# Optimization experiments

Hardware: AMD Instinct MI355X
Metric: run time of the kernel (lower is better)

The kernel has to match this reference:

```python
import jax, jax.numpy as jnp
import numpy as np

DIM = 4096
N_HEAD = 32
N_KV_HEAD = 8
HEAD_DIM = DIM // N_HEAD  # 128
B, T = 2, 2048


def _rope_freqs(T, head_dim, theta=10000.0):
    inv = 1.0 / (theta ** (np.arange(0, head_dim, 2, dtype=np.float32) / head_dim))
    t = np.arange(T, dtype=np.float32)
    ang = np.outer(t, inv)  # [T, head_dim/2]
    return jnp.asarray(np.stack([np.cos(ang), np.sin(ang)], axis=-1))  # [T, hd/2, 2]


def setup_inputs() -> dict:
    key = jax.random.key(0)
    ks = jax.random.split(key, 5)
    s = 1.0 / np.sqrt(DIM)
    return {
        "x": jax.random.normal(ks[0], (B, T, DIM), dtype=jnp.float32),
        "freqs_cis": _rope_freqs(T, HEAD_DIM),
        "wq": jax.random.normal(ks[1], (DIM, N_HEAD * HEAD_DIM), dtype=jnp.float32) * s,
        "wk": jax.random.normal(ks[2], (DIM, N_KV_HEAD * HEAD_DIM), dtype=jnp.float32) * s,
        "wv": jax.random.normal(ks[3], (DIM, N_KV_HEAD * HEAD_DIM), dtype=jnp.float32) * s,
        "wo": jax.random.normal(ks[4], (DIM, DIM), dtype=jnp.float32) * s,
    }


def _apply_rotary(x, freqs_cis):
    # x: [B, T, H, head_dim]; freqs_cis: [T, head_dim/2, 2]
    xs = x.reshape(*x.shape[:-1], -1, 2)  # [B, T, H, hd/2, 2]
    fc = freqs_cis[None, :, None, :, :]   # [1, T, 1, hd/2, 2]
    real = xs[..., 0] * fc[..., 0] - xs[..., 1] * fc[..., 1]
    imag = xs[..., 1] * fc[..., 0] + xs[..., 0] * fc[..., 1]
    return jnp.stack([real, imag], axis=-1).reshape(x.shape)


def reference(x, freqs_cis, wq, wk, wv, wo):
    Bx, Tx, C = x.shape
    q = (x @ wq).reshape(Bx, Tx, N_HEAD, HEAD_DIM)
    k = (x @ wk).reshape(Bx, Tx, N_KV_HEAD, HEAD_DIM)
    v = (x @ wv).reshape(Bx, Tx, N_KV_HEAD, HEAD_DIM)
    q = _apply_rotary(q, freqs_cis)
    k = _apply_rotary(k, freqs_cis)
    # [B, H, T, hd]
    q = q.transpose(0, 2, 1, 3)
    k = k.transpose(0, 2, 1, 3)
    v = v.transpose(0, 2, 1, 3)
    # GQA: expand kv heads to match query heads
    rep = N_HEAD // N_KV_HEAD
    k = jnp.repeat(k, rep, axis=1)
    v = jnp.repeat(v, rep, axis=1)
    scale = 1.0 / np.sqrt(HEAD_DIM)
    scores = jnp.einsum("bhqd,bhkd->bhqk", q, k) * scale
    causal = jnp.tril(jnp.ones((Tx, Tx), dtype=bool))
    scores = jnp.where(causal[None, None], scores, jnp.float32(-1e30))
    attn = jax.nn.softmax(scores, axis=-1)
    y = jnp.einsum("bhqk,bhkd->bhqd", attn, v)
    y = y.transpose(0, 2, 1, 3).reshape(Bx, Tx, C)
    return y @ wo
```

## Files before the change

### kernel.cpp

```cpp
#include <hip/hip_runtime.h>

#define DIM  4096
#define NH   32
#define NKV  8
#define HD   128
#define BSZ  2
#define TSEQ 2048

typedef __bf16 bf16x8 __attribute__((ext_vector_type(8)));
typedef unsigned short ushort8v __attribute__((ext_vector_type(8)));
typedef float f32x4 __attribute__((ext_vector_type(4)));

typedef void GV __attribute__((address_space(1)));
typedef void LV __attribute__((address_space(3)));

__device__ __forceinline__ unsigned short f2bf(float f) {
  unsigned u = __builtin_bit_cast(unsigned, f);
  u += 0x7FFFu + ((u >> 16) & 1u);
  return (unsigned short)(u >> 16);
}
__device__ __forceinline__ float bf2f(unsigned short b) {
  unsigned u = ((unsigned)b) << 16;
  return __builtin_bit_cast(float, u);
}
__device__ __forceinline__ void gload16(const unsigned short* g, unsigned short* l) {
  __builtin_amdgcn_global_load_lds((GV*)g, (LV*)l, 16, 0, 0);
}
__device__ __forceinline__ f32x4 mfma16(bf16x8 a, bf16x8 b, f32x4 c) {
  return __builtin_amdgcn_mfma_f32_16x16x32_bf16(a, b, c, 0, 0, 0);
}
__device__ __forceinline__ bf16x8 lds8(const unsigned short* p) {
  return __builtin_bit_cast(bf16x8, *(const ushort8v*)p);
}

__global__ void detect_dtype(const unsigned int* __restrict__ fc, int* __restrict__ flag) {
  if (threadIdx.x == 0 && blockIdx.x == 0)
    *flag = (fc[0] == 0x3F800000u) ? 0 : 1;
}

__global__ void cast_x(const void* __restrict__ src, unsigned short* __restrict__ dst,
                       const int* __restrict__ flag) {
  long t = (long)blockIdx.x * 256 + threadIdx.x;
  if (*flag) {
    ((uint2*)dst)[t] = ((const uint2*)src)[t];
  } else {
    float4 f = ((const float4*)src)[t];
    ushort4 o;
    o.x = f2bf(f.x); o.y = f2bf(f.y); o.z = f2bf(f.z); o.w = f2bf(f.w);
    ((ushort4*)dst)[t] = o;
  }
}

__global__ __launch_bounds__(256) void transpose64(const void* __restrict__ src,
                                                   unsigned short* __restrict__ dst,
                                                   int R, int C, const int* __restrict__ flag) {
  __shared__ unsigned short tile[64][68];
  const int isbf = *flag;
  const int tid = threadIdx.x;
  const int c0g = blockIdx.x * 64, r0g = blockIdx.y * 64;
  const int cc = (tid & 15) * 4;
  if (isbf) {
    const unsigned short* s = (const unsigned short*)src;
#pragma unroll
    for (int it = 0; it < 4; ++it) {
      const int r = it * 16 + (tid >> 4);
      ushort4 v = *(const ushort4*)(s + (long)(r0g + r) * C + c0g + cc);
      *(ushort4*)&tile[r][cc] = v;
    }
  } else {
    const float* s = (const float*)src;
#pragma unroll
    for (int it = 0; it < 4; ++it) {
      const int r = it * 16 + (tid >> 4);
      float4 f = *(const float4*)(s + (long)(r0g + r) * C + c0g + cc);
      ushort4 v;
      v.x = f2bf(f.x); v.y = f2bf(f.y); v.z = f2bf(f.z); v.w = f2bf(f.w);
      *(ushort4*)&tile[r][cc] = v;
    }
  }
  __syncthreads();
#pragma unroll
  for (int it = 0; it < 2; ++it) {
    const int c = (tid >> 3) + it * 32;
    const int r0 = (tid & 7) * 8;
    ushort8v o;
#pragma unroll
    for (int u = 0; u < 8; ++u) o[u] = tile[r0 + u][c];
    *(ushort8v*)(dst + (long)(c0g + c) * R + r0g + r0) = o;
  }
}

__device__ __forceinline__ void gemm256_loop(const unsigned short* __restrict__ A,
                                             const unsigned short* __restrict__ Bt,
                                             unsigned short* As, unsigned short* Bs,
                                             long tileM, long tileN, f32x4 (&acc)[8][4]) {
  const int tid = (int)threadIdx.x;
  const int lane = tid & 63, wave = tid >> 6;
  const int wr = wave >> 2, wc = wave & 3;
  const int lm = lane & 15, quad = lane >> 4;
  const int srow = wave * 8 + (lane >> 3);
  const int schunk = ((lane & 7) ^ (lane >> 3)) * 8;
  const unsigned short* Ag = A + (tileM + srow) * 4096L + schunk;
  const unsigned short* Bg = Bt + (tileN + srow) * 4096L + schunk;
  unsigned short* Al = As + srow * 64 + (lane & 7) * 8;
  unsigned short* Bl = Bs + srow * 64 + (lane & 7) * 8;

  auto stgA = [&](int slot, int h, int tt) {
    const unsigned short* g = Ag + (long)h * 524288L + (long)tt * 64;
    unsigned short* l = Al + slot * 16384 + h * 8192;
    gload16(g, l);
    gload16(g + 262144L, l + 4096);
  };
  auto stgB = [&](int slot, int h, int tt) {
    const unsigned short* g = Bg + (long)h * 524288L + (long)tt * 64;
    unsigned short* l = Bl + slot * 16384 + h * 8192;
    gload16(g, l);
    gload16(g + 262144L, l + 4096);
  };
  auto rdA = [&](int so, int f16, int kk) {
    return lds8(&As[so + (wr * 128 + f16 * 16 + lm) * 64 + (((kk * 4 + quad) ^ (lm & 7)) * 8)]);
  };
  auto rdB = [&](int so, int f16, int kk) {
    return lds8(&Bs[so + (wc * 64 + f16 * 16 + lm) * 64 + (((kk * 4 + quad) ^ (lm & 7)) * 8)]);
  };

  stgB(0, 0, 0); stgB(0, 1, 0); stgA(0, 0, 0); stgA(0, 1, 0);
  stgB(1, 0, 1); stgB(1, 1, 1); stgA(1, 0, 1);
  asm volatile("s_waitcnt vmcnt(6)" ::: "memory");
  __builtin_amdgcn_sched_barrier(0);
  __builtin_amdgcn_s_barrier();
  __builtin_amdgcn_sched_barrier(0);

#pragma unroll 2
  for (int t = 0; t < 64; ++t) {
    const int s = t & 1;
    const int so = s * 16384;
    bf16x8 a[4][2], b[4][2];
#pragma unroll
    for (int f = 0; f < 4; ++f) { a[f][0] = rdA(so, f, 0); a[f][1] = rdA(so, f, 1); }
#pragma unroll
    for (int f = 0; f < 4; ++f) { b[f][0] = rdB(so, f, 0); b[f][1] = rdB(so, f, 1); }
    if (t < 63) stgA(s ^ 1, 1, t + 1);
    __builtin_amdgcn_sched_barrier(0);
    __builtin_amdgcn_s_barrier();
    asm volatile("s_waitcnt lgkmcnt(0)" ::: "memory");
    __builtin_amdgcn_sched_barrier(0);
    __builtin_amdgcn_s_setprio(1);
#pragma unroll
    for (int mf = 0; mf < 4; ++mf)
#pragma unroll
      for (int nf = 0; nf < 2; ++nf) {
        acc[mf][nf] = mfma16(a[mf][0], b[nf][0], acc[mf][nf]);
        acc[mf][nf] = mfma16(a[mf][1], b[nf][1], acc[mf][nf]);
      }
    __builtin_amdgcn_s_setprio(0);
    __builtin_amdgcn_sched_barrier(0);
    __builtin_amdgcn_s_barrier();
    if (t < 62) stgB(s, 0, t + 2);
    __builtin_amdgcn_sched_barrier(0);
    __builtin_amdgcn_s_barrier();
    __builtin_amdgcn_sched_barrier(0);
    __builtin_amdgcn_s_setprio(1);
#pragma unroll
    for (int mf = 0; mf < 4; ++mf)
#pragma unroll
      for (int nf = 2; nf < 4; ++nf) {
        acc[mf][nf] = mfma16(a[mf][0], b[nf][0], acc[mf][nf]);
        acc[mf][nf] = mfma16(a[mf][1], b[nf][1], acc[mf][nf]);
      }
    __builtin_amdgcn_s_setprio(0);
    __builtin_amdgcn_sched_barrier(0);
    __builtin_amdgcn_s_barrier();
#pragma unroll
    for (int f = 0; f < 4; ++f) { a[f][0] = rdA(so, f + 4, 0); a[f][1] = rdA(so, f + 4, 1); }
    if (t < 62) stgB(s, 1, t + 2);
    __builtin_amdgcn_sched_barrier(0);
    __builtin_amdgcn_s_barrier();
    asm volatile("s_waitcnt lgkmcnt(0)" ::: "memory");
    __builtin_amdgcn_sched_barrier(0);
    __builtin_amdgcn_s_setprio(1);
#pragma unroll
    for (int mf = 0; mf < 4; ++mf)
#pragma unroll
      for (int nf = 0; nf < 2; ++nf) {
        acc[mf + 4][nf] = mfma16(a[mf][0], b[nf][0], acc[mf + 4][nf]);
        acc[mf + 4][nf] = mfma16(a[mf][1], b[nf][1], acc[mf + 4][nf]);
      }
    __builtin_amdgcn_s_setprio(0);
    __builtin_amdgcn_sched_barrier(0);
    __builtin_amdgcn_s_barrier();
    if (t < 62) stgA(s, 0, t + 2);
    __builtin_amdgcn_sched_barrier(0);
    __builtin_amdgcn_s_barrier();
    __builtin_amdgcn_sched_barrier(0);
    __builtin_amdgcn_s_setprio(1);
#pragma unroll
    for (int mf = 0; mf < 4; ++mf)
#pragma unroll
      for (int nf = 2; nf < 4; ++nf) {
        acc[mf + 4][nf] = mfma16(a[mf][0], b[nf][0], acc[mf + 4][nf]);
        acc[mf + 4][nf] = mfma16(a[mf][1], b[nf][1], acc[mf + 4][nf]);
      }
    __builtin_amdgcn_s_setprio(0);
    if (t < 62)       asm volatile("s_waitcnt vmcnt(6)" ::: "memory");
    else if (t == 62) asm volatile("s_waitcnt vmcnt(0)" ::: "memory");
    __builtin_amdgcn_sched_barrier(0);
    __builtin_amdgcn_s_barrier();
  }
}

__global__ __launch_bounds__(512, 2) void gemm_qkv8(const unsigned short* __restrict__ A,
                                                    const unsigned short* __restrict__ Bt,
                                                    const void* __restrict__ fcv,
                                                    const int* __restrict__ flag,
                                                    unsigned short* __restrict__ qo,
                                                    unsigned short* __restrict__ ko,
                                                    unsigned short* __restrict__ vo) {
  __shared__ __align__(16) unsigned short As[2 * 16384];
  __shared__ __align__(16) unsigned short Bs[2 * 16384];
  const int bid = (int)blockIdx.x;
  const int nb2 = (bid & 7) * 48 + (bid >> 3);
  const long tileM = (long)(nb2 / 24) * 256;
  const long tileN = (long)(nb2 % 24) * 256;
  f32x4 acc[8][4] = {};
  gemm256_loop(A, Bt, As, Bs, tileM, tileN, acc);
  const int tid = (int)threadIdx.x;
  const int lane = tid & 63, wave = tid >> 6;
  const int wr = wave >> 2, wc = wave & 3;
  const int lm = lane & 15, quad = lane >> 4;
  const int isbf = *flag;
  const int nb = (int)tileN + wc * 64;
  if (nb < 5120) {
    const int isk = (nb >= 4096);
    unsigned short* dst = isk ? ko : qo;
    const int hpb = isk ? NKV : NH;
    const int coff = isk ? 4096 : 0;
#pragma unroll
    for (int mf = 0; mf < 8; ++mf)
#pragma unroll
      for (int r = 0; r < 4; ++r) {
        const int m = (int)tileM + wr * 128 + mf * 16 + quad * 4 + r;
        const int b = m >> 11, tq = m & (TSEQ - 1);
#pragma unroll
        for (int nf = 0; nf < 4; ++nf) {
          const int n = nb + nf * 16 + lm;
          float val = acc[mf][nf][r];
          float par = __shfl_xor(val, 1);
          const int ip = (n & 127) >> 1;
          const long fo = (long)tq * 64 + ip;
          float cz, sz;
          if (isbf) {
            const unsigned short* fu = (const unsigned short*)fcv;
            cz = bf2f(fu[fo * 2]); sz = bf2f(fu[fo * 2 + 1]);
          } else {
            float2 cs = ((const float2*)fcv)[fo];
            cz = cs.x; sz = cs.y;
          }
          float out = (n & 1) ? (val * cz + par * sz) : (val * cz - par * sz);
          const int h = (n - coff) >> 7, d = n & 127;
          dst[((long)(b * hpb + h) * TSEQ + tq) * HD + d] = f2bf(out);
        }
      }
  } else {
#pragma unroll
    for (int mf = 0; mf < 8; ++mf)
#pragma unroll
      for (int r = 0; r < 4; ++r) {
        const int m = (int)tileM + wr * 128 + mf * 16 + quad * 4 + r;
        const int b = m >> 11, tq = m & (TSEQ - 1);
#pragma unroll
        for (int nf = 0; nf < 4; ++nf) {
          const int n = nb + nf * 16 + lm;
          const int h = (n - 5120) >> 7, d = n & 127;
          vo[((long)(b * NKV + h) * HD + d) * TSEQ + tq] = f2bf(acc[mf][nf][r]);
        }
      }
  }
}

__global__ __launch_bounds__(512, 2) void gemm_wo8(const unsigned short* __restrict__ A,
                                                   const unsigned short* __restrict__ Bt,
                                                   void* __restrict__ Cv,
                                                   const int* __restrict__ flag) {
  __shared__ __align__(16) unsigned short As[2 * 16384];
  __shared__ __align__(16) unsigned short Bs[2 * 16384];
  const int bid = (int)blockIdx.x;
  const int nb2 = (bid & 7) * 32 + (bid >> 3);
  const long tileM = (long)(nb2 >> 4) * 256;
  const long tileN = (long)(nb2 & 15) * 256;
  f32x4 acc[8][4] = {};
  gemm256_loop(A, Bt, As, Bs, tileM, tileN, acc);
  const int tid = (int)threadIdx.x;
  const int lane = tid & 63, wave = tid >> 6;
  const int wr = wave >> 2, wc = wave & 3;
  const int lm = lane & 15, quad = lane >> 4;
  const int obf = *flag;
  const long N = 4096;
  if (obf) {
    unsigned short* C = (unsigned short*)Cv;
#pragma unroll
    for (int mf = 0; mf < 8; ++mf)
#pragma unroll
      for (int nf = 0; nf < 4; ++nf)
#pragma unroll
        for (int r = 0; r < 4; ++r)
          C[(tileM + wr * 128 + mf * 16 + quad * 4 + r) * N + tileN + wc * 64 + nf * 16 + lm] =
              f2bf(acc[mf][nf][r]);
  } else {
    float* C = (float*)Cv;
#pragma unroll
    for (int mf = 0; mf < 8; ++mf)
#pragma unroll
      for (int nf = 0; nf < 4; ++nf)
#pragma unroll
        for (int r = 0; r < 4; ++r)
          C[(tileM + wr * 128 + mf * 16 + quad * 4 + r) * N + tileN + wc * 64 + nf * 16 + lm] =
              acc[mf][nf][r];
  }
}

__global__ __launch_bounds__(256, 3) void flash_attn(const unsigned short* __restrict__ q,
                                                     const unsigned short* __restrict__ k,
                                                     const unsigned short* __restrict__ vT,
                                                     unsigned short* __restrict__ y) {
  __shared__ unsigned short Ks[2][32 * 128];
  __shared__ unsigned short Vs[2][128 * 32];
  __shared__ unsigned short Pl[4][32 * 40];
  const int tid = threadIdx.x;
  const int lane = tid & 63, wave = tid >> 6;
  const int lm = lane & 15, quad = lane >> 4;
  const int bh = blockIdx.y, b = bh >> 5, h = bh & 31, kvh = h >> 2;
  const int qi = (int)gridDim.x - 1 - (int)blockIdx.x;
  const int q0 = qi * 128;
  const unsigned short* Qb = q + ((long)(b * NH + h) * TSEQ + q0 + wave * 32) * HD;
  const unsigned short* Kb = k + (long)(b * NKV + kvh) * TSEQ * HD;
  const unsigned short* Vb = vT + (long)(b * NKV + kvh) * HD * TSEQ;
  bf16x8 qf[2][4];
#pragma unroll
  for (int mi = 0; mi < 2; ++mi)
#pragma unroll
    for (int ks = 0; ks < 4; ++ks)
      qf[mi][ks] = __builtin_bit_cast(bf16x8,
          *(const ushort8v*)(Qb + (mi * 16 + lm) * HD + ks * 32 + quad * 8));
  f32x4 o[2][8] = {};
  float li[2][4] = {};
  const float scale = 0.08838834764831845f;
  const int krow = tid >> 4, kcl = ((tid & 15) ^ (krow & 7)) * 8;
  const int vrow = tid >> 2, vcl = ((tid & 3) ^ ((vrow >> 1) & 3)) * 8;
  const int ktiles = qi * 4 + 4;
  {
    gload16(Kb + krow * HD + kcl, &Ks[0][tid * 8]);
    gload16(Kb + (16 + krow) * HD + kcl, &Ks[0][2048 + tid * 8]);
    gload16(Vb + (long)vrow * TSEQ + vcl, &Vs[0][tid * 8]);
    gload16(Vb + (long)(64 + vrow) * TSEQ + vcl, &Vs[0][2048 + tid * 8]);
  }
  for (int kt = 0; kt < ktiles; ++kt) {
    __syncthreads();
    if (kt + 1 < ktiles) {
      const int bi = (kt + 1) & 1;
      const unsigned short* Kg = Kb + (long)(kt + 1) * 32 * HD;
      gload16(Kg + krow * HD + kcl, &Ks[bi][tid * 8]);
      gload16(Kg + (16 + krow) * HD + kcl, &Ks[bi][2048 + tid * 8]);
      const unsigned short* Vg = Vb + (kt + 1) * 32;
      gload16(Vg + (long)vrow * TSEQ + vcl, &Vs[bi][tid * 8]);
      gload16(Vg + (long)(64 + vrow) * TSEQ + vcl, &Vs[bi][2048 + tid * 8]);
    }
    const unsigned short* KsB = Ks[kt & 1];
    const unsigned short* VsB = Vs[kt & 1];
    f32x4 s[2][2] = {};
#pragma unroll
    for (int ni = 0; ni < 2; ++ni)
#pragma unroll
      for (int ks = 0; ks < 4; ++ks) {
        bf16x8 kf = lds8(&KsB[(ni * 16 + lm) * 128 + ((ks * 4 + quad) ^ (lm & 7)) * 8]);
        s[0][ni] = mfma16(qf[0][ks], kf, s[0][ni]);
        s[1][ni] = mfma16(qf[1][ks], kf, s[1][ni]);
      }
    unsigned short* PlW = &Pl[wave][0];
#pragma unroll
    for (int mi = 0; mi < 2; ++mi)
#pragma unroll
      for (int r = 0; r < 4; ++r) {
        const int qg = q0 + wave * 32 + mi * 16 + quad * 4 + r;
#pragma unroll
        for (int ni = 0; ni < 2; ++ni) {
          const int kg = kt * 32 + ni * 16 + lm;
          float p = (kg <= qg) ? __expf(s[mi][ni][r] * scale) : 0.f;
          li[mi][r] += p;
          PlW[(mi * 16 + quad * 4 + r) * 40 + ni * 16 + lm] = f2bf(p);
        }
      }
    bf16x8 pf0 = lds8(&PlW[lm * 40 + quad * 8]);
    bf16x8 pf1 = lds8(&PlW[(16 + lm) * 40 + quad * 8]);
#pragma unroll
    for (int db = 0; db < 8; ++db) {
      bf16x8 vf = lds8(&VsB[(db * 16 + lm) * 32 + (quad ^ ((lm >> 1) & 3)) * 8]);
      o[0][db] = mfma16(pf0, vf, o[0][db]);
      o[1][db] = mfma16(pf1, vf, o[1][db]);
    }
  }
  float inv[2][4];
#pragma unroll
  for (int mi = 0; mi < 2; ++mi)
#pragma unroll
    for (int r = 0; r < 4; ++r) {
      float l = li[mi][r];
      l += __shfl_xor(l, 1, 16);
      l += __shfl_xor(l, 2, 16);
      l += __shfl_xor(l, 4, 16);
      l += __shfl_xor(l, 8, 16);
      inv[mi][r] = 1.0f / l;
    }
  unsigned short* yo = y + ((long)b * TSEQ + q0 + wave * 32) * DIM + h * 128 + lm;
#pragma unroll
  for (int mi = 0; mi < 2; ++mi)
#pragma unroll
    for (int r = 0; r < 4; ++r) {
      unsigned short* yr = yo + (long)(mi * 16 + quad * 4 + r) * DIM;
#pragma unroll
      for (int db = 0; db < 8; ++db)
        yr[db * 16] = f2bf(o[mi][db][r] * inv[mi][r]);
    }
}

extern "C" void kernel_launch(void* const* d_in, const int* in_sizes, int n_in,
                              void* d_out, int out_size, void* d_ws, size_t ws_size,
                              hipStream_t stream) {
  const void* x  = d_in[0];
  const void* fc = d_in[1];
  const void* wq = d_in[2];
  const void* wk = d_in[3];
  const void* wv = d_in[4];
  const void* wo = d_in[5];
  char* ws = (char*)d_ws;
  int* flag             = (int*)ws;
  unsigned short* xb    = (unsigned short*)(ws + 256);
  unsigned short* wqkvT = xb + 16777216L;
  unsigned short* woT   = wqkvT + 25165824L;
  unsigned short* qb    = woT + 16777216L;
  unsigned short* kb    = qb + 16777216L;
  unsigned short* vb    = kb + 4194304L;
  unsigned short* yb    = xb;

  detect_dtype<<<dim3(1), dim3(64), 0, stream>>>((const unsigned int*)fc, flag);
  cast_x<<<dim3(16384), dim3(256), 0, stream>>>(x, xb, flag);
  transpose64<<<dim3(64, 64), dim3(256), 0, stream>>>(wq, wqkvT, 4096, 4096, flag);
  transpose64<<<dim3(16, 64), dim3(256), 0, stream>>>(wk, wqkvT + 4096L * 4096, 4096, 1024, flag);
  transpose64<<<dim3(16, 64), dim3(256), 0, stream>>>(wv, wqkvT + 5120L * 4096, 4096, 1024, flag);
  transpose64<<<dim3(64, 64), dim3(256), 0, stream>>>(wo, woT, 4096, 4096, flag);
  gemm_qkv8<<<dim3(384), dim3(512), 0, stream>>>(xb, wqkvT, fc, flag, qb, kb, vb);
  flash_attn<<<dim3(16, 64), dim3(256), 0, stream>>>(qb, kb, vb, yb);
  gemm_wo8<<<dim3(256), dim3(512), 0, stream>>>(yb, woT, d_out, flag);
}
```

Measured before the change: 831.5 us.

## Split B-fragment LDS reads across quadrants and drop sched barriers in QKV GEMM loop

Reworks the main GEMM k-loop so the B fragments are read from LDS in two halves, each just before the MFMA quadrant that uses it. The global stage of B-half-1 and A-half-0 is merged into a single phase. Explicit lgkmcnt waits and most sched_barrier fences are removed, leaving the compiler to insert waits and schedule freely. The aim is to overlap LDS reads with MFMA work and cut register pressure and barrier overhead. The risk is that the compiler's scheduling is worse than the hand-fenced version.

```diff
diff --git a/kernel.cpp b/kernel.cpp
--- a/kernel.cpp
+++ b/kernel.cpp
@@ -127,84 +127,70 @@
   stgB(0, 0, 0); stgB(0, 1, 0); stgA(0, 0, 0); stgA(0, 1, 0);
   stgB(1, 0, 1); stgB(1, 1, 1); stgA(1, 0, 1);
   asm volatile("s_waitcnt vmcnt(6)" ::: "memory");
-  __builtin_amdgcn_sched_barrier(0);
   __builtin_amdgcn_s_barrier();
-  __builtin_amdgcn_sched_barrier(0);
 
 #pragma unroll 2
   for (int t = 0; t < 64; ++t) {
+    __builtin_amdgcn_sched_barrier(0);
     const int s = t & 1;
     const int so = s * 16384;
-    bf16x8 a[4][2], b[4][2];
+    bf16x8 a[4][2], b0[2][2], b1[2][2];
 #pragma unroll
     for (int f = 0; f < 4; ++f) { a[f][0] = rdA(so, f, 0); a[f][1] = rdA(so, f, 1); }
 #pragma unroll
-    for (int f = 0; f < 4; ++f) { b[f][0] = rdB(so, f, 0); b[f][1] = rdB(so, f, 1); }
+    for (int f = 0; f < 2; ++f) { b0[f][0] = rdB(so, f, 0); b0[f][1] = rdB(so, f, 1); }
     if (t < 63) stgA(s ^ 1, 1, t + 1);
-    __builtin_amdgcn_sched_barrier(0);
-    __builtin_amdgcn_s_barrier();
-    asm volatile("s_waitcnt lgkmcnt(0)" ::: "memory");
-    __builtin_amdgcn_sched_barrier(0);
+    __builtin_amdgcn_s_barrier();
     __builtin_amdgcn_s_setprio(1);
 #pragma unroll
     for (int mf = 0; mf < 4; ++mf)
 #pragma unroll
       for (int nf = 0; nf < 2; ++nf) {
-        acc[mf][nf] = mfma16(a[mf][0], b[nf][0], acc[mf][nf]);
-        acc[mf][nf] = mfma16(a[mf][1], b[nf][1], acc[mf][nf]);
+        acc[mf][nf] = mfma16(a[mf][0], b0[nf][0], acc[mf][nf]);
+        acc[mf][nf] = mfma16(a[mf][1], b0[nf][1], acc[mf][nf]);
       }
     __builtin_amdgcn_s_setprio(0);
-    __builtin_amdgcn_sched_barrier(0);
-    __builtin_amdgcn_s_barrier();
+    __builtin_amdgcn_s_barrier();
+#pragma unroll
+    for (int f = 0; f < 2; ++f) { b1[f][0] = rdB(so, f + 2, 0); b1[f][1] = rdB(so, f + 2, 1); }
+    __builtin_amdgcn_s_barrier();
+    __builtin_amdgcn_s_setprio(1);
+#pragma unroll
+    for (int mf = 0; mf < 4; ++mf)
+#pragma unroll
+      for (int nf = 0; nf < 2; ++nf) {
+        acc[mf][nf + 2] = mfma16(a[mf][0], b1[nf][0], acc[mf][nf + 2]);
+        acc[mf][nf + 2] = mfma16(a[mf][1], b1[nf][1], acc[mf][nf + 2]);
+      }
+    __builtin_amdgcn_s_setprio(0);
+    __builtin_amdgcn_s_barrier();
+#pragma unroll
+    for (int f = 0; f < 4; ++f) { a[f][0] = rdA(so, f + 4, 0); a[f][1] = rdA(so, f + 4, 1); }
     if (t < 62) stgB(s, 0, t + 2);
-    __builtin_amdgcn_sched_barrier(0);
-    __builtin_amdgcn_s_barrier();
-    __builtin_amdgcn_sched_barrier(0);
+    __builtin_amdgcn_s_barrier();
     __builtin_amdgcn_s_setprio(1);
 #pragma unroll
     for (int mf = 0; mf < 4; ++mf)
 #pragma unroll
-      for (int nf = 2; nf < 4; ++nf) {
-        acc[mf][nf] = mfma16(a[mf][0], b[nf][0], acc[mf][nf]);
-        acc[mf][nf] = mfma16(a[mf][1], b[nf][1], acc[mf][nf]);
+      for (int nf = 0; nf < 2; ++nf) {
+        acc[mf + 4][nf] = mfma16(a[mf][0], b0[nf][0], acc[mf + 4][nf]);
+        acc[mf + 4][nf] = mfma16(a[mf][1], b0[nf][1], acc[mf + 4][nf]);
       }
     __builtin_amdgcn_s_setprio(0);
-    __builtin_amdgcn_sched_barrier(0);
-    __builtin_amdgcn_s_barrier();
-#pragma unroll
-    for (int f = 0; f < 4; ++f) { a[f][0] = rdA(so, f + 4, 0); a[f][1] = rdA(so, f + 4, 1); }
-    if (t < 62) stgB(s, 1, t + 2);
-    __builtin_amdgcn_sched_barrier(0);
-    __builtin_amdgcn_s_barrier();
-    asm volatile("s_waitcnt lgkmcnt(0)" ::: "memory");
-    __builtin_amdgcn_sched_barrier(0);
+    __builtin_amdgcn_s_barrier();
+    if (t < 62) { stgB(s, 1, t + 2); stgA(s, 0, t + 2); }
+    __builtin_amdgcn_s_barrier();
     __builtin_amdgcn_s_setprio(1);
 #pragma unroll
     for (int mf = 0; mf < 4; ++mf)
 #pragma unroll
       for (int nf = 0; nf < 2; ++nf) {
-        acc[mf + 4][nf] = mfma16(a[mf][0], b[nf][0], acc[mf + 4][nf]);
-        acc[mf + 4][nf] = mfma16(a[mf][1], b[nf][1], acc[mf + 4][nf]);
-      }
-    __builtin_amdgcn_s_setprio(0);
-    __builtin_amdgcn_sched_barrier(0);
-    __builtin_amdgcn_s_barrier();
-    if (t < 62) stgA(s, 0, t + 2);
-    __builtin_amdgcn_sched_barrier(0);
-    __builtin_amdgcn_s_barrier();
-    __builtin_amdgcn_sched_barrier(0);
-    __builtin_amdgcn_s_setprio(1);
-#pragma unroll
-    for (int mf = 0; mf < 4; ++mf)
-#pragma unroll
-      for (int nf = 2; nf < 4; ++nf) {
-        acc[mf + 4][nf] = mfma16(a[mf][0], b[nf][0], acc[mf + 4][nf]);
-        acc[mf + 4][nf] = mfma16(a[mf][1], b[nf][1], acc[mf + 4][nf]);
+        acc[mf + 4][nf + 2] = mfma16(a[mf][0], b1[nf][0], acc[mf + 4][nf + 2]);
+        acc[mf + 4][nf + 2] = mfma16(a[mf][1], b1[nf][1], acc[mf + 4][nf + 2]);
       }
     __builtin_amdgcn_s_setprio(0);
     if (t < 62)       asm volatile("s_waitcnt vmcnt(6)" ::: "memory");
     else if (t == 62) asm volatile("s_waitcnt vmcnt(0)" ::: "memory");
-    __builtin_amdgcn_sched_barrier(0);
     __builtin_amdgcn_s_barrier();
   }
 }
```

Measured after the change: 846.0 us. Within noise of the previous version (+1.7%).

## Shrink GEMM tiles from 256x256 to 128x128 with 4-wave blocks

Applied to the files above, without the earlier changes.

Replaces the 256x256, 512-thread GEMM main loop with a 128x128, 256-thread version and halves the LDS buffers. The QKV and output projection GEMMs now launch four times as many blocks, and the block-index swizzles and epilogue indexing are updated to match. The aim is better CU occupancy and load balance (384/256 blocks on a 256-CU part). The cost is lower arithmetic intensity per tile, so more global and LDS traffic per FLOP, plus more barriers per MFMA.

```diff
diff --git a/kernel.cpp b/kernel.cpp
--- a/kernel.cpp
+++ b/kernel.cpp
@@ -90,38 +90,38 @@
   }
 }
 
-__device__ __forceinline__ void gemm256_loop(const unsigned short* __restrict__ A,
+__device__ __forceinline__ void gemm128_loop(const unsigned short* __restrict__ A,
                                              const unsigned short* __restrict__ Bt,
                                              unsigned short* As, unsigned short* Bs,
-                                             long tileM, long tileN, f32x4 (&acc)[8][4]) {
+                                             long tileM, long tileN, f32x4 (&acc)[4][4]) {
   const int tid = (int)threadIdx.x;
   const int lane = tid & 63, wave = tid >> 6;
-  const int wr = wave >> 2, wc = wave & 3;
+  const int wr = wave >> 1, wc = wave & 1;
   const int lm = lane & 15, quad = lane >> 4;
-  const int srow = wave * 8 + (lane >> 3);
-  const int schunk = ((lane & 7) ^ (lane >> 3)) * 8;
-  const unsigned short* Ag = A + (tileM + srow) * 4096L + schunk;
-  const unsigned short* Bg = Bt + (tileN + srow) * 4096L + schunk;
-  unsigned short* Al = As + srow * 64 + (lane & 7) * 8;
-  unsigned short* Bl = Bs + srow * 64 + (lane & 7) * 8;
-
-  auto stgA = [&](int slot, int h, int tt) {
-    const unsigned short* g = Ag + (long)h * 524288L + (long)tt * 64;
-    unsigned short* l = Al + slot * 16384 + h * 8192;
+  const int sr = tid >> 3;
+  const int schunk = ((tid & 7) ^ (sr & 7)) * 8;
+  const unsigned short* Ag = A + (tileM + sr) * 4096L + schunk;
+  const unsigned short* Bg = Bt + (tileN + sr) * 4096L + schunk;
+  unsigned short* Al = As + sr * 64 + (tid & 7) * 8;
+  unsigned short* Bl = Bs + sr * 64 + (tid & 7) * 8;
+
+  auto stgA = [&](int slot, int half, int tt) {
+    const unsigned short* g = Ag + (long)half * (64 * 4096L) + (long)tt * 64;
+    unsigned short* l = Al + slot * 8192 + half * 4096;
     gload16(g, l);
-    gload16(g + 262144L, l + 4096);
+    gload16(g + 32 * 4096L, l + 2048);
   };
-  auto stgB = [&](int slot, int h, int tt) {
-    const unsigned short* g = Bg + (long)h * 524288L + (long)tt * 64;
-    unsigned short* l = Bl + slot * 16384 + h * 8192;
+  auto stgB = [&](int slot, int half, int tt) {
+    const unsigned short* g = Bg + (long)half * (64 * 4096L) + (long)tt * 64;
+    unsigned short* l = Bl + slot * 8192 + half * 4096;
     gload16(g, l);
-    gload16(g + 262144L, l + 4096);
+    gload16(g + 32 * 4096L, l + 2048);
   };
-  auto rdA = [&](int so, int f16, int kk) {
-    return lds8(&As[so + (wr * 128 + f16 * 16 + lm) * 64 + (((kk * 4 + quad) ^ (lm & 7)) * 8)]);
+  auto rdA = [&](int so, int f, int kk) {
+    return lds8(&As[so + (wr * 64 + f * 16 + lm) * 64 + (((kk * 4 + quad) ^ (lm & 7)) * 8)]);
   };
-  auto rdB = [&](int so, int f16, int kk) {
-    return lds8(&Bs[so + (wc * 64 + f16 * 16 + lm) * 64 + (((kk * 4 + quad) ^ (lm & 7)) * 8)]);
+  auto rdB = [&](int so, int f, int kk) {
+    return lds8(&Bs[so + (wc * 64 + f * 16 + lm) * 64 + (((kk * 4 + quad) ^ (lm & 7)) * 8)]);
   };
 
   stgB(0, 0, 0); stgB(0, 1, 0); stgA(0, 0, 0); stgA(0, 1, 0);
@@ -129,12 +129,12 @@
   asm volatile("s_waitcnt vmcnt(6)" ::: "memory");
   __builtin_amdgcn_sched_barrier(0);
   __builtin_amdgcn_s_barrier();
-  __builtin_amdgcn_sched_barrier(0);
 
 #pragma unroll 2
   for (int t = 0; t < 64; ++t) {
+    __builtin_amdgcn_sched_barrier(0);
     const int s = t & 1;
-    const int so = s * 16384;
+    const int so = s * 8192;
     bf16x8 a[4][2], b[4][2];
 #pragma unroll
     for (int f = 0; f < 4; ++f) { a[f][0] = rdA(so, f, 0); a[f][1] = rdA(so, f, 1); }
@@ -149,14 +149,38 @@
 #pragma unroll
     for (int mf = 0; mf < 4; ++mf)
 #pragma unroll
-      for (int nf = 0; nf < 2; ++nf) {
+      for (int nf = 0; nf < 2; ++nf)
         acc[mf][nf] = mfma16(a[mf][0], b[nf][0], acc[mf][nf]);
+    __builtin_amdgcn_s_setprio(0);
+    __builtin_amdgcn_sched_barrier(0);
+    __builtin_amdgcn_s_barrier();
+    if (t < 62) stgB(s, 0, t + 2);
+    __builtin_amdgcn_sched_barrier(0);
+    __builtin_amdgcn_s_barrier();
+    __builtin_amdgcn_sched_barrier(0);
+    __builtin_amdgcn_s_setprio(1);
+#pragma unroll
+    for (int mf = 0; mf < 4; ++mf)
+#pragma unroll
+      for (int nf = 0; nf < 2; ++nf)
+        acc[mf][nf + 2] = mfma16(a[mf][0], b[nf + 2][0], acc[mf][nf + 2]);
+    __builtin_amdgcn_s_setprio(0);
+    __builtin_amdgcn_sched_barrier(0);
+    __builtin_amdgcn_s_barrier();
+    if (t < 62) stgB(s, 1, t + 2);
+    __builtin_amdgcn_sched_barrier(0);
+    __builtin_amdgcn_s_barrier();
+    __builtin_amdgcn_sched_barrier(0);
+    __builtin_amdgcn_s_setprio(1);
+#pragma unroll
+    for (int mf = 0; mf < 4; ++mf)
+#pragma unroll
+      for (int nf = 0; nf < 2; ++nf)
         acc[mf][nf] = mfma16(a[mf][1], b[nf][1], acc[mf][nf]);
-      }
     __builtin_amdgcn_s_setprio(0);
     __builtin_amdgcn_sched_barrier(0);
     __builtin_amdgcn_s_barrier();
-    if (t < 62) stgB(s, 0, t + 2);
+    if (t < 62) stgA(s, 0, t + 2);
     __builtin_amdgcn_sched_barrier(0);
     __builtin_amdgcn_s_barrier();
     __builtin_amdgcn_sched_barrier(0);
@@ -164,43 +188,8 @@
 #pragma unroll
     for (int mf = 0; mf < 4; ++mf)
 #pragma unroll
-      for (int nf = 2; nf < 4; ++nf) {
-        acc[mf][nf] = mfma16(a[mf][0], b[nf][0], acc[mf][nf]);
-        acc[mf][nf] = mfma16(a[mf][1], b[nf][1], acc[mf][nf]);
-      }
-    __builtin_amdgcn_s_setprio(0);
-    __builtin_amdgcn_sched_barrier(0);
-    __builtin_amdgcn_s_barrier();
-#pragma unroll
-    for (int f = 0; f < 4; ++f) { a[f][0] = rdA(so, f + 4, 0); a[f][1] = rdA(so, f + 4, 1); }
-    if (t < 62) stgB(s, 1, t + 2);
-    __builtin_amdgcn_sched_barrier(0);
-    __builtin_amdgcn_s_barrier();
-    asm volatile("s_waitcnt lgkmcnt(0)" ::: "memory");
-    __builtin_amdgcn_sched_barrier(0);
-    __builtin_amdgcn_s_setprio(1);
-#pragma unroll
-    for (int mf = 0; mf < 4; ++mf)
-#pragma unroll
-      for (int nf = 0; nf < 2; ++nf) {
-        acc[mf + 4][nf] = mfma16(a[mf][0], b[nf][0], acc[mf + 4][nf]);
-        acc[mf + 4][nf] = mfma16(a[mf][1], b[nf][1], acc[mf + 4][nf]);
-      }
-    __builtin_amdgcn_s_setprio(0);
-    __builtin_amdgcn_sched_barrier(0);
-    __builtin_amdgcn_s_barrier();
-    if (t < 62) stgA(s, 0, t + 2);
-    __builtin_amdgcn_sched_barrier(0);
-    __builtin_amdgcn_s_barrier();
-    __builtin_amdgcn_sched_barrier(0);
-    __builtin_amdgcn_s_setprio(1);
-#pragma unroll
-    for (int mf = 0; mf < 4; ++mf)
-#pragma unroll
-      for (int nf = 2; nf < 4; ++nf) {
-        acc[mf + 4][nf] = mfma16(a[mf][0], b[nf][0], acc[mf + 4][nf]);
-        acc[mf + 4][nf] = mfma16(a[mf][1], b[nf][1], acc[mf + 4][nf]);
-      }
+      for (int nf = 0; nf < 2; ++nf)
+        acc[mf][nf + 2] = mfma16(a[mf][1], b[nf + 2][1], acc[mf][nf + 2]);
     __builtin_amdgcn_s_setprio(0);
     if (t < 62)       asm volatile("s_waitcnt vmcnt(6)" ::: "memory");
     else if (t == 62) asm volatile("s_waitcnt vmcnt(0)" ::: "memory");
@@ -209,24 +198,24 @@
   }
 }
 
-__global__ __launch_bounds__(512, 2) void gemm_qkv8(const unsigned short* __restrict__ A,
+__global__ __launch_bounds__(256, 2) void gemm_qkv8(const unsigned short* __restrict__ A,
                                                     const unsigned short* __restrict__ Bt,
                                                     const void* __restrict__ fcv,
                                                     const int* __restrict__ flag,
                                                     unsigned short* __restrict__ qo,
                                                     unsigned short* __restrict__ ko,
                                                     unsigned short* __restrict__ vo) {
-  __shared__ __align__(16) unsigned short As[2 * 16384];
-  __shared__ __align__(16) unsigned short Bs[2 * 16384];
+  __shared__ __align__(16) unsigned short As[2 * 8192];
+  __shared__ __align__(16) unsigned short Bs[2 * 8192];
   const int bid = (int)blockIdx.x;
-  const int nb2 = (bid & 7) * 48 + (bid >> 3);
-  const long tileM = (long)(nb2 / 24) * 256;
-  const long tileN = (long)(nb2 % 24) * 256;
-  f32x4 acc[8][4] = {};
-  gemm256_loop(A, Bt, As, Bs, tileM, tileN, acc);
+  const int nb2 = (bid & 7) * 192 + (bid >> 3);
+  const long tileM = (long)(nb2 / 48) * 128;
+  const long tileN = (long)(nb2 % 48) * 128;
+  f32x4 acc[4][4] = {};
+  gemm128_loop(A, Bt, As, Bs, tileM, tileN, acc);
   const int tid = (int)threadIdx.x;
   const int lane = tid & 63, wave = tid >> 6;
-  const int wr = wave >> 2, wc = wave & 3;
+  const int wr = wave >> 1, wc = wave & 1;
   const int lm = lane & 15, quad = lane >> 4;
   const int isbf = *flag;
   const int nb = (int)tileN + wc * 64;
@@ -236,10 +225,10 @@
     const int hpb = isk ? NKV : NH;
     const int coff = isk ? 4096 : 0;
 #pragma unroll
-    for (int mf = 0; mf < 8; ++mf)
+    for (int mf = 0; mf < 4; ++mf)
 #pragma unroll
       for (int r = 0; r < 4; ++r) {
-        const int m = (int)tileM + wr * 128 + mf * 16 + quad * 4 + r;
+        const int m = (int)tileM + wr * 64 + mf * 16 + quad * 4 + r;
         const int b = m >> 11, tq = m & (TSEQ - 1);
 #pragma unroll
         for (int nf = 0; nf < 4; ++nf) {
@@ -263,10 +252,10 @@
       }
   } else {
 #pragma unroll
-    for (int mf = 0; mf < 8; ++mf)
+    for (int mf = 0; mf < 4; ++mf)
 #pragma unroll
       for (int r = 0; r < 4; ++r) {
-        const int m = (int)tileM + wr * 128 + mf * 16 + quad * 4 + r;
+        const int m = (int)tileM + wr * 64 + mf * 16 + quad * 4 + r;
         const int b = m >> 11, tq = m & (TSEQ - 1);
 #pragma unroll
         for (int nf = 0; nf < 4; ++nf) {
@@ -278,43 +267,43 @@
   }
 }
 
-__global__ __launch_bounds__(512, 2) void gemm_wo8(const unsigned short* __restrict__ A,
+__global__ __launch_bounds__(256, 2) void gemm_wo8(const unsigned short* __restrict__ A,
                                                    const unsigned short* __restrict__ Bt,
                                                    void* __restrict__ Cv,
                                                    const int* __restrict__ flag) {
-  __shared__ __align__(16) unsigned short As[2 * 16384];
-  __shared__ __align__(16) unsigned short Bs[2 * 16384];
+  __shared__ __align__(16) unsigned short As[2 * 8192];
+  __shared__ __align__(16) unsigned short Bs[2 * 8192];
   const int bid = (int)blockIdx.x;
-  const int nb2 = (bid & 7) * 32 + (bid >> 3);
-  const long tileM = (long)(nb2 >> 4) * 256;
-  const long tileN = (long)(nb2 & 15) * 256;
-  f32x4 acc[8][4] = {};
-  gemm256_loop(A, Bt, As, Bs, tileM, tileN, acc);
+  const int nb2 = (bid & 7) * 128 + (bid >> 3);
+  const long tileM = (long)(nb2 >> 5) * 128;
+  const long tileN = (long)(nb2 & 31) * 128;
+  f32x4 acc[4][4] = {};
+  gemm128_loop(A, Bt, As, Bs, tileM, tileN, acc);
   const int tid = (int)threadIdx.x;
   const int lane = tid & 63, wave = tid >> 6;
-  const int wr = wave >> 2, wc = wave & 3;
+  const int wr = wave >> 1, wc = wave & 1;
   const int lm = lane & 15, quad = lane >> 4;
   const int obf = *flag;
   const long N = 4096;
   if (obf) {
     unsigned short* C = (unsigned short*)Cv;
 #pragma unroll
-    for (int mf = 0; mf < 8; ++mf)
+    for (int mf = 0; mf < 4; ++mf)
 #pragma unroll
       for (int nf = 0; nf < 4; ++nf)
 #pragma unroll
         for (int r = 0; r < 4; ++r)
-          C[(tileM + wr * 128 + mf * 16 + quad * 4 + r) * N + tileN + wc * 64 + nf * 16 + lm] =
+          C[(tileM + wr * 64 + mf * 16 + quad * 4 + r) * N + tileN + wc * 64 + nf * 16 + lm] =
               f2bf(acc[mf][nf][r]);
   } else {
     float* C = (float*)Cv;
 #pragma unroll
-    for (int mf = 0; mf < 8; ++mf)
+    for (int mf = 0; mf < 4; ++mf)
 #pragma unroll
       for (int nf = 0; nf < 4; ++nf)
 #pragma unroll
         for (int r = 0; r < 4; ++r)
-          C[(tileM + wr * 128 + mf * 16 + quad * 4 + r) * N + tileN + wc * 64 + nf * 16 + lm] =
+          C[(tileM + wr * 64 + mf * 16 + quad * 4 + r) * N + tileN + wc * 64 + nf * 16 + lm] =
               acc[mf][nf][r];
   }
 }
@@ -448,7 +437,7 @@
   transpose64<<<dim3(16, 64), dim3(256), 0, stream>>>(wk, wqkvT + 4096L * 4096, 4096, 1024, flag);
   transpose64<<<dim3(16, 64), dim3(256), 0, stream>>>(wv, wqkvT + 5120L * 4096, 4096, 1024, flag);
   transpose64<<<dim3(64, 64), dim3(256), 0, stream>>>(wo, woT, 4096, 4096, flag);
-  gemm_qkv8<<<dim3(384), dim3(512), 0, stream>>>(xb, wqkvT, fc, flag, qb, kb, vb);
+  gemm_qkv8<<<dim3(1536), dim3(256), 0, stream>>>(xb, wqkvT, fc, flag, qb, kb, vb);
   flash_attn<<<dim3(16, 64), dim3(256), 0, stream>>>(qb, kb, vb, yb);
-  gemm_wo8<<<dim3(256), dim3(512), 0, stream>>>(yb, woT, d_out, flag);
-}
+  gemm_wo8<<<dim3(1024), dim3(256), 0, stream>>>(yb, woT, d_out, flag);
+}
```

Result: no change. 846.3 us (+1.8%).
